# Kernel tuning notes

Measured on AMD Instinct MI355X. Metric: run time of the kernel, lower is better.

Reference implementation:

```python
import jax, jax.numpy as jnp
import numpy as np

NUM_HEADS = 16
HEAD_DIM = 64
NUM_BUCKETS = 32
MAX_DIST = 128
EPS = 1e-5
SCALE = HEAD_DIM ** -0.5


def layer_norm(x, g, b):
    m = jnp.mean(x, axis=-1, keepdims=True)
    v = jnp.mean(jnp.square(x - m), axis=-1, keepdims=True)
    return (x - m) * jax.lax.rsqrt(v + EPS) * g + b


def rel_pos_bias(emb, num_q, num_k):
    # T5-style relative position bucketing (non-causal, bidirectional halves)
    i, j = num_q, num_k
    q_pos = jnp.arange(j - i, j)
    k_pos = jnp.arange(j)
    rel = k_pos[None, :] - q_pos[:, None]  # [i, j]
    nb = NUM_BUCKETS // 2
    ret = (rel >= 0).astype(jnp.int32) * nb
    n = jnp.abs(rel)
    max_exact = nb // 2
    val_large = max_exact + (
        jnp.log(jnp.maximum(n, 1).astype(jnp.float32) / max_exact)
        / np.log(MAX_DIST / max_exact) * (nb - max_exact)
    ).astype(jnp.int32)
    val_large = jnp.minimum(val_large, nb - 1)
    bucket = ret + jnp.where(n < max_exact, n, val_large)
    bias = emb[bucket]                       # [i, j, h]
    return jnp.transpose(bias, (2, 0, 1))[None]  # [1, h, i, j]


def attention(x, ctx, ng, nbv, ncg, ncb, wq, wkv, wo, bo, rel_emb):
    b, n, _ = x.shape
    m = ctx.shape[1]
    xn = layer_norm(x, ng, nbv)
    cn = layer_norm(ctx, ncg, ncb)
    q = xn @ wq                              # [b, n, mid]
    kv = cn @ wkv                            # [b, m, 2*mid]
    k, v = jnp.split(kv, 2, axis=-1)
    def heads(t, L):
        return t.reshape(b, L, NUM_HEADS, HEAD_DIM).transpose(0, 2, 1, 3)
    q, k, v = heads(q, n), heads(k, m), heads(v, m)
    sim = jnp.einsum('bhnd,bhmd->bhnm', q, k)
    sim = (sim + rel_pos_bias(rel_emb, n, m)) * SCALE  # bias added pre-scale (faithful)
    attn = jax.nn.softmax(sim, axis=-1)
    out = jnp.einsum('bhnm,bhmd->bhnd', attn, v)
    out = out.transpose(0, 2, 1, 3).reshape(b, n, NUM_HEADS * HEAD_DIM)
    return out @ wo + bo


def setup_inputs() -> dict:
    key = jax.random.key(0)
    ks = jax.random.split(key, 20)
    F, MID, CF = 1024, NUM_HEADS * HEAD_DIM, 1024
    w = lambda k, shape, s=0.02: jax.random.normal(k, shape, jnp.float32) * s
    inp = {
        'x': jax.random.normal(ks[0], (2, 2048, F), jnp.float32),
        'context': jax.random.normal(ks[1], (2, 512, CF), jnp.float32),
        # self-attention params
        'sa_norm_g': 1.0 + w(ks[2], (F,), 0.1), 'sa_norm_b': w(ks[3], (F,), 0.1),
        'sa_normc_g': 1.0 + w(ks[4], (F,), 0.1), 'sa_normc_b': w(ks[5], (F,), 0.1),
        'sa_wq': w(ks[6], (F, MID)), 'sa_wkv': w(ks[7], (F, 2 * MID)),
        'sa_wo': w(ks[8], (MID, F)), 'sa_bo': w(ks[9], (F,), 0.01),
        'sa_rel': w(ks[10], (NUM_BUCKETS, NUM_HEADS), 0.1),
        # cross-attention params
        'ca_norm_g': 1.0 + w(ks[11], (F,), 0.1), 'ca_norm_b': w(ks[12], (F,), 0.1),
        'ca_normc_g': 1.0 + w(ks[13], (CF,), 0.1), 'ca_normc_b': w(ks[14], (CF,), 0.1),
        'ca_wq': w(ks[15], (F, MID)), 'ca_wkv': w(ks[16], (CF, 2 * MID)),
        'ca_wo': w(ks[17], (MID, F)), 'ca_bo': w(ks[18], (F,), 0.01),
        'ca_rel': w(ks[19], (NUM_BUCKETS, NUM_HEADS), 0.1),
    }
    return inp


def reference(x, context,
              sa_norm_g, sa_norm_b, sa_normc_g, sa_normc_b,
              sa_wq, sa_wkv, sa_wo, sa_bo, sa_rel,
              ca_norm_g, ca_norm_b, ca_normc_g, ca_normc_b,
              ca_wq, ca_wkv, ca_wo, ca_bo, ca_rel):
    # self-attention (context = x, norm_context applied to x)
    x = attention(x, x, sa_norm_g, sa_norm_b, sa_normc_g, sa_normc_b,
                  sa_wq, sa_wkv, sa_wo, sa_bo, sa_rel) + x
    # cross-attention with residual
    x = attention(x, context, ca_norm_g, ca_norm_b, ca_normc_g, ca_normc_b,
                  ca_wq, ca_wkv, ca_wo, ca_bo, ca_rel) + x
    return x
```

## Files before the change

kernel.cpp:

```cpp
#include <hip/hip_runtime.h>
#include <hip/hip_bf16.h>

typedef __hip_bfloat16 bf16;
typedef __attribute__((ext_vector_type(8))) short bf16x8;
typedef __attribute__((ext_vector_type(4))) float f32x4;

__device__ __forceinline__ float b2f(bf16 v) { return __bfloat162float(v); }
__device__ __forceinline__ bf16 f2b(float v) { return __float2bfloat16(v); }

__device__ __forceinline__ float ldx(const void* p, size_t i, bool isb) {
    return isb ? b2f(((const bf16*)p)[i]) : ((const float*)p)[i];
}
__device__ __forceinline__ void stx(void* p, size_t i, bool isb, float v) {
    if (isb) ((bf16*)p)[i] = f2b(v);
    else     ((float*)p)[i] = v;
}
__device__ __forceinline__ void ldx8(const void* p, size_t i, bool isb, float* o) {
    if (isb) {
        const bf16x8 v = *(const bf16x8*)((const bf16*)p + i);
#pragma unroll
        for (int j = 0; j < 8; j++) o[j] = b2f(((const bf16*)&v)[j]);
    } else {
        const float4 v0 = *(const float4*)((const float*)p + i);
        const float4 v1 = *(const float4*)((const float*)p + i + 4);
        o[0]=v0.x; o[1]=v0.y; o[2]=v0.z; o[3]=v0.w;
        o[4]=v1.x; o[5]=v1.y; o[6]=v1.z; o[7]=v1.w;
    }
}

__global__ void sniff_kernel(const void* __restrict__ x, int* __restrict__ flag) {
    const unsigned* w = (const unsigned*)x;
    const int t = threadIdx.x;
    int cnt = 0;
#pragma unroll
    for (int i = 0; i < 4; i++) {
        const unsigned word = w[t * 4 + i];
        const int e = (word >> 23) & 0xFF;
        cnt += (e >= 192) ? 1 : 0;
    }
    __shared__ int red[4];
#pragma unroll
    for (int o = 32; o > 0; o >>= 1) cnt += __shfl_down(cnt, o);
    if ((t & 63) == 0) red[t >> 6] = cnt;
    __syncthreads();
    if (t == 0) flag[0] = ((red[0] + red[1] + red[2] + red[3]) >= 512) ? 1 : 0;
}

__global__ void wconv4_kernel(const void* __restrict__ Wq,
                              const void* __restrict__ Wkv,
                              const void* __restrict__ Wo,
                              bf16* __restrict__ WTq, bf16* __restrict__ WTkv,
                              bf16* __restrict__ WTo,
                              const int* __restrict__ flagp) {
    const bool isb = (*flagp != 0);
    const int z = blockIdx.z;
    const void* W = (z == 0) ? Wq : (z == 3) ? Wo : Wkv;
    bf16* Wt      = (z == 0) ? WTq : (z == 3) ? WTo : WTkv;
    const int N   = (z == 1 || z == 2) ? 2048 : 1024;
    const int K = 1024;
    __shared__ float T[64][65];
    const int n0 = blockIdx.x * 64 + ((z == 2) ? 1024 : 0);
    const int k0 = blockIdx.y * 64;
    const int t = threadIdx.x;
    const int rr = t >> 3, c8 = (t & 7) * 8;
#pragma unroll
    for (int i = 0; i < 2; i++) {
        const int row = rr + i * 32;
        float v[8];
        ldx8(W, (size_t)(k0 + row) * N + n0 + c8, isb, v);
#pragma unroll
        for (int j = 0; j < 8; j++) T[row][c8 + j] = v[j];
    }
    __syncthreads();
#pragma unroll
    for (int i = 0; i < 2; i++) {
        const int row = rr + i * 32;
        bf16x8 ov;
#pragma unroll
        for (int j = 0; j < 8; j++) ((bf16*)&ov)[j] = f2b(T[c8 + j][row]);
        *(bf16x8*)(Wt + (size_t)(n0 + row) * K + k0 + c8) = ov;
    }
}

__global__ void ln_dual_kernel(const void* __restrict__ in, size_t in_off, long in_bs,
                               int in_ext,
                               const void* __restrict__ g1, const void* __restrict__ b1,
                               const void* __restrict__ g2, const void* __restrict__ b2,
                               bf16* __restrict__ out1, bf16* __restrict__ out2,
                               long out_bs, const int* __restrict__ flagp) {
    const int F = 1024;
    const bool isb = (*flagp != 0);
    const bool inb = in_ext ? isb : true;
    const int row = blockIdx.x;
    const int z = blockIdx.z;
    const int t = threadIdx.x;
    const size_t base = in_off + (size_t)z * in_bs + (size_t)row * F;
    const size_t obase = (size_t)z * out_bs + (size_t)row * F;

    float v[4];
    float s = 0.f;
#pragma unroll
    for (int i = 0; i < 4; i++) { v[i] = ldx(in, base + t + 256 * i, inb); s += v[i]; }

    __shared__ float red1[4];
    __shared__ float red2[4];
#pragma unroll
    for (int o = 32; o > 0; o >>= 1) s += __shfl_down(s, o);
    if ((t & 63) == 0) red1[t >> 6] = s;
    __syncthreads();
    const float mean = (red1[0] + red1[1] + red1[2] + red1[3]) * (1.0f / F);

    float ss = 0.f;
#pragma unroll
    for (int i = 0; i < 4; i++) { float d = v[i] - mean; ss += d * d; }
#pragma unroll
    for (int o = 32; o > 0; o >>= 1) ss += __shfl_down(ss, o);
    if ((t & 63) == 0) red2[t >> 6] = ss;
    __syncthreads();
    const float var = (red2[0] + red2[1] + red2[2] + red2[3]) * (1.0f / F);
    const float rn = rsqrtf(var + 1e-5f);

#pragma unroll
    for (int i = 0; i < 4; i++) {
        const int idx = t + 256 * i;
        const float nv = (v[i] - mean) * rn;
        out1[obase + idx] = f2b(nv * ldx(g1, idx, isb) + ldx(b1, idx, isb));
        if (out2) out2[obase + idx] = f2b(nv * ldx(g2, idx, isb) + ldx(b2, idx, isb));
    }
}

__global__ __launch_bounds__(256) void gemm_bt(
    const bf16* __restrict__ A, const bf16* __restrict__ Bt,
    void* __restrict__ C, int c_ext,
    const void* __restrict__ bias,
    const void* __restrict__ res, int res_ext,
    int N, int mode, int zsplit, int zrows,
    bf16* __restrict__ kb0, bf16* __restrict__ kb1,
    const int* __restrict__ flagp) {

    const int K = 1024;
    const bool isb = (*flagp != 0);

    __shared__ bf16 As[128][72];
    __shared__ bf16 Bs[128][72];

    const int t = threadIdx.x;
    const int w = t >> 6, lane = t & 63, li = lane & 15, quad = lane >> 4;
    const int wm = (w & 1) * 64, wn = (w >> 1) * 64;
    const int bm = blockIdx.y * 128, bn = blockIdx.x * 128;

    f32x4 acc[4][4];
#pragma unroll
    for (int mi = 0; mi < 4; mi++)
#pragma unroll
        for (int ni = 0; ni < 4; ni++)
#pragma unroll
            for (int r = 0; r < 4; r++) acc[mi][ni][r] = 0.f;

    for (int k0 = 0; k0 < K; k0 += 64) {
#pragma unroll
        for (int c = 0; c < 4; c++) {
            const int d = c * 256 + t;
            const int row = d >> 3, ch = (d & 7) * 8;
            *(bf16x8*)&As[row][ch] = *(const bf16x8*)(A + (size_t)(bm + row) * K + k0 + ch);
            *(bf16x8*)&Bs[row][ch] = *(const bf16x8*)(Bt + (size_t)(bn + row) * K + k0 + ch);
        }
        __syncthreads();
#pragma unroll
        for (int kc = 0; kc < 2; kc++) {
            bf16x8 af[4], bfr[4];
#pragma unroll
            for (int i = 0; i < 4; i++) {
                af[i]  = *(const bf16x8*)&As[wm + i * 16 + li][kc * 32 + quad * 8];
                bfr[i] = *(const bf16x8*)&Bs[wn + i * 16 + li][kc * 32 + quad * 8];
            }
#pragma unroll
            for (int mi = 0; mi < 4; mi++)
#pragma unroll
                for (int ni = 0; ni < 4; ni++)
                    acc[mi][ni] = __builtin_amdgcn_mfma_f32_16x16x32_bf16(
                        af[mi], bfr[ni], acc[mi][ni], 0, 0, 0);
        }
        __syncthreads();
    }

    if (mode == 1) {
#pragma unroll
        for (int mi = 0; mi < 4; mi++)
#pragma unroll
            for (int r = 0; r < 4; r++) {
                const int row = bm + wm + mi * 16 + quad * 4 + r;
                bf16* kb = (row < zsplit) ? kb0 : kb1;
                const int lrow = (row < zsplit) ? row : row - zsplit;
#pragma unroll
                for (int ni = 0; ni < 4; ni++) {
                    const int col = bn + wn + ni * 16 + li;
                    const float v = acc[mi][ni][r];
                    if (col < 1024)
                        kb[(size_t)lrow * 1024 + col] = f2b(v);
                    else
                        kb[(size_t)1024 * zrows + (size_t)(col - 1024) * zrows + lrow] = f2b(v);
                }
            }
        return;
    }

#pragma unroll
    for (int mi = 0; mi < 4; mi++)
#pragma unroll
        for (int r = 0; r < 4; r++) {
            const int row = bm + wm + mi * 16 + quad * 4 + r;
#pragma unroll
            for (int ni = 0; ni < 4; ni++) {
                const int col = bn + wn + ni * 16 + li;
                float v = acc[mi][ni][r];
                if (bias) v += ldx(bias, col, isb);
                if (res)  v += ldx(res, (size_t)row * N + col, res_ext ? isb : true);
                stx(C, (size_t)row * N + col, c_ext ? isb : true, v);
            }
        }
}

__global__ __launch_bounds__(256) void gemm_mfma(
    const bf16* __restrict__ A, long a_bs, const void* __restrict__ W,
    void* __restrict__ C, size_t c_off, long c_bs, int c_ext,
    const void* __restrict__ bias,
    const void* __restrict__ res, size_t res_off, long res_bs, int res_ext,
    int K, int N, int mode, int R,
    bf16* __restrict__ kb0, bf16* __restrict__ kb1,
    const int* __restrict__ flagp) {

    const bool isb = (*flagp != 0);
    const bool resb = res_ext ? isb : true;
    const bool cb = c_ext ? isb : true;
    const int z = blockIdx.z;

    const bf16* Az = A + (size_t)z * a_bs;
    const size_t coz = c_off + (size_t)z * c_bs;
    const size_t roz = res_off + (size_t)z * res_bs;

    __shared__ bf16 As[64][72];
    __shared__ bf16 Bs[64][72];

    const int t = threadIdx.x;
    const int w = t >> 6, lane = t & 63, li = lane & 15, quad = lane >> 4;
    const int wm = (w & 1) * 32, wn = (w >> 1) * 32;
    const int bm = blockIdx.y * 64, bn = blockIdx.x * 64;

    f32x4 acc[2][2];
#pragma unroll
    for (int mi = 0; mi < 2; mi++)
#pragma unroll
        for (int ni = 0; ni < 2; ni++)
#pragma unroll
            for (int r = 0; r < 4; r++) acc[mi][ni][r] = 0.f;

    for (int k0 = 0; k0 < K; k0 += 64) {
#pragma unroll
        for (int c = 0; c < 2; c++) {
            const int lin = t * 16 + c * 8;
            const int row = lin >> 6, kk = lin & 63;
            *(bf16x8*)&As[row][kk] = *(const bf16x8*)(Az + (size_t)(bm + row) * K + k0 + kk);
        }
#pragma unroll
        for (int c = 0; c < 2; c++) {
            const int lin = t * 16 + c * 8;
            const int kk = lin >> 6, n0 = lin & 63;
            float v[8];
            ldx8(W, (size_t)(k0 + kk) * N + bn + n0, isb, v);
            const int st = t & 7;
#pragma unroll
            for (int i = 0; i < 8; i++) {
                const int ii = (i + st) & 7;
                Bs[n0 + ii][kk] = f2b(v[ii]);
            }
        }
        __syncthreads();
#pragma unroll
        for (int kc = 0; kc < 2; kc++) {
            bf16x8 af[2], bfr[2];
#pragma unroll
            for (int mi = 0; mi < 2; mi++)
                af[mi] = *(const bf16x8*)&As[wm + mi * 16 + li][kc * 32 + quad * 8];
#pragma unroll
            for (int ni = 0; ni < 2; ni++)
                bfr[ni] = *(const bf16x8*)&Bs[wn + ni * 16 + li][kc * 32 + quad * 8];
#pragma unroll
            for (int mi = 0; mi < 2; mi++)
#pragma unroll
                for (int ni = 0; ni < 2; ni++)
                    acc[mi][ni] = __builtin_amdgcn_mfma_f32_16x16x32_bf16(
                        af[mi], bfr[ni], acc[mi][ni], 0, 0, 0);
        }
        __syncthreads();
    }

    if (mode == 1) {
        bf16* kb = z ? kb1 : kb0;
#pragma unroll
        for (int mi = 0; mi < 2; mi++)
#pragma unroll
            for (int r = 0; r < 4; r++) {
                const int row = bm + wm + mi * 16 + quad * 4 + r;
#pragma unroll
                for (int ni = 0; ni < 2; ni++) {
                    const int col = bn + wn + ni * 16 + li;
                    const float v = acc[mi][ni][r];
                    if (col < 1024)
                        kb[(size_t)row * 1024 + col] = f2b(v);
                    else
                        kb[(size_t)1024 * R + (size_t)(col - 1024) * R + row] = f2b(v);
                }
            }
        return;
    }

#pragma unroll
    for (int mi = 0; mi < 2; mi++)
#pragma unroll
        for (int r = 0; r < 4; r++) {
            const int row = bm + wm + mi * 16 + quad * 4 + r;
#pragma unroll
            for (int ni = 0; ni < 2; ni++) {
                const int col = bn + wn + ni * 16 + li;
                float v = acc[mi][ni][r];
                if (bias) v += ldx(bias, col, isb);
                if (res)  v += ldx(res, roz + (size_t)row * N + col, resb);
                stx(C, coz + (size_t)row * N + col, cb, v);
            }
        }
}

__global__ __launch_bounds__(64) void attn_flash(
    const bf16* __restrict__ qb, const bf16* __restrict__ kv0,
    const bf16* __restrict__ kv1,
    const void* __restrict__ rel_emb, bf16* __restrict__ out,
    long qo_bs, long out_bs, int m, int rel_off, const int* __restrict__ flagp) {

    const float SC = 0.125f * 1.44269504f;
    const bool isb = (*flagp != 0);
    const int id = blockIdx.x;
    const int xcd = id & 7;
    const int slot = id >> 3;
    const int c = (slot >> 6) * 8 + xcd;
    const int h = c & 15, z = c >> 4;
    const int q0 = (slot & 63) * 32;
    const int t = threadIdx.x;
    const int li = t & 15, quad = t >> 4;

    const bf16* qz = qb + (size_t)z * qo_bs;
    bf16* oz = out + (size_t)z * out_bs;
    const bf16* kb = z ? kv1 : kv0;
    const bf16* vtb = kb + (size_t)m * 1024;

    __shared__ float bias_s[32];
    __shared__ float tab[2080];
    __shared__ bf16 Ps[16][40];

    if (t < 32) bias_s[t] = ldx(rel_emb, t * 16 + h, isb) * SC - 40.0f;
    __syncthreads();

    const int tsz = m + 31;
    for (int i = t; i < tsz; i += 64) {
        const int rel = i - 31 - q0 + rel_off;
        const int ab = rel < 0 ? -rel : rel;
        int bucket = rel >= 0 ? 16 : 0;
        if (ab < 8) {
            bucket += ab;
        } else {
            const int p = 31 - __clz(ab);
            const int k2 = 2 * p + ((ab * ab >= (1 << (2 * p + 1))) ? 1 : 0);
            const int val = k2 + 2;
            bucket += (val > 15) ? 15 : val;
        }
        tab[i] = bias_s[bucket];
    }
    __syncthreads();

    bf16x8 aq[2][2];
#pragma unroll
    for (int g = 0; g < 2; g++)
#pragma unroll
        for (int kc = 0; kc < 2; kc++)
            aq[g][kc] = *(const bf16x8*)(qz + (size_t)(q0 + g * 16 + li) * 1024
                                         + h * 64 + kc * 32 + quad * 8);

    bf16x8 ones;
#pragma unroll
    for (int j = 0; j < 8; j++) ((short*)&ones)[j] = 0x3F80;

    f32x4 o[2][4], lac[2];
#pragma unroll
    for (int g = 0; g < 2; g++) {
#pragma unroll
        for (int r = 0; r < 4; r++) lac[g][r] = 0.f;
#pragma unroll
        for (int nb = 0; nb < 4; nb++)
#pragma unroll
            for (int r = 0; r < 4; r++) o[g][nb][r] = 0.f;
    }

    for (int j0 = 0; j0 < m; j0 += 32) {
        bf16x8 kf[4], vf[4];
#pragma unroll
        for (int nb = 0; nb < 2; nb++)
#pragma unroll
            for (int kc = 0; kc < 2; kc++)
                kf[nb * 2 + kc] = *(const bf16x8*)(
                    kb + (size_t)(j0 + nb * 16 + li) * 1024 + h * 64 + kc * 32 + quad * 8);
#pragma unroll
        for (int nb = 0; nb < 4; nb++)
            vf[nb] = *(const bf16x8*)(
                vtb + (size_t)(h * 64 + nb * 16 + li) * m + j0 + quad * 8);

#pragma unroll
        for (int g = 0; g < 2; g++) {
            f32x4 s[2];
#pragma unroll
            for (int nb = 0; nb < 2; nb++) {
                f32x4 a;
#pragma unroll
                for (int r = 0; r < 4; r++) a[r] = 0.f;
#pragma unroll
                for (int kc = 0; kc < 2; kc++)
                    a = __builtin_amdgcn_mfma_f32_16x16x32_bf16(aq[g][kc], kf[nb * 2 + kc],
                                                                a, 0, 0, 0);
                s[nb] = a;
            }
#pragma unroll
            for (int nb = 0; nb < 2; nb++)
#pragma unroll
                for (int r = 0; r < 4; r++) {
                    const int ti = j0 + nb * 16 + li + 31 - (g * 16 + quad * 4 + r);
                    s[nb][r] = exp2f(fmaf(s[nb][r], SC, tab[ti]));
                }
#pragma unroll
            for (int nb = 0; nb < 2; nb++)
#pragma unroll
                for (int r = 0; r < 4; r++)
                    Ps[quad * 4 + r][nb * 16 + li] = f2b(s[nb][r]);
            const bf16x8 ap = *(const bf16x8*)&Ps[li][quad * 8];
#pragma unroll
            for (int nb = 0; nb < 4; nb++)
                o[g][nb] = __builtin_amdgcn_mfma_f32_16x16x32_bf16(ap, vf[nb],
                                                                   o[g][nb], 0, 0, 0);
            lac[g] = __builtin_amdgcn_mfma_f32_16x16x32_bf16(ap, ones, lac[g], 0, 0, 0);
        }
    }

#pragma unroll
    for (int g = 0; g < 2; g++)
#pragma unroll
        for (int r = 0; r < 4; r++) {
            const float inv = 1.0f / lac[g][r];
            const int qi = q0 + g * 16 + quad * 4 + r;
#pragma unroll
            for (int nb = 0; nb < 4; nb++)
                oz[(size_t)qi * 1024 + h * 64 + nb * 16 + li] = f2b(o[g][nb][r] * inv);
        }
}

extern "C" void kernel_launch(void* const* d_in, const int* in_sizes, int n_in,
                              void* d_out, int out_size, void* d_ws, size_t ws_size,
                              hipStream_t stream) {
    const long M1 = 1024 * 1024;
    const long M2 = 2 * 1024 * 1024;
    const long M4 = 4 * 1024 * 1024;
    if (ws_size < 24u * 1024 * 1024 + 256) return;

    const void* x      = d_in[0];
    const void* ctx    = d_in[1];
    const void* sa_ng  = d_in[2];
    const void* sa_nb  = d_in[3];
    const void* sa_ncg = d_in[4];
    const void* sa_ncb = d_in[5];
    const void* sa_wq  = d_in[6];
    const void* sa_wkv = d_in[7];
    const void* sa_wo  = d_in[8];
    const void* sa_bo  = d_in[9];
    const void* sa_rel = d_in[10];
    const void* ca_ng  = d_in[11];
    const void* ca_nb  = d_in[12];
    const void* ca_ncg = d_in[13];
    const void* ca_ncb = d_in[14];
    const void* ca_wq  = d_in[15];
    const void* ca_wkv = d_in[16];
    const void* ca_wo  = d_in[17];
    const void* ca_bo  = d_in[18];
    const void* ca_rel = d_in[19];

    int* flag = (int*)d_ws;
    bf16* F_A = (bf16*)((char*)d_ws + 256);
    bf16* F_B = F_A + M4;
    bf16* F_C = F_B + M4;
    bf16* WT  = F_C + M4;
    bf16* qd  = (bf16*)d_out;

    sniff_kernel<<<1, 256, 0, stream>>>(x, flag);

    if (ws_size >= 32u * 1024 * 1024 + 256) {
        bf16* WTq = WT;
        bf16* WTkv = WT + M1;
        bf16* WTo = WT + 3 * M1;

        wconv4_kernel<<<dim3(16, 16, 4), 256, 0, stream>>>(
            sa_wq, sa_wkv, sa_wo, WTq, WTkv, WTo, flag);
        ln_dual_kernel<<<dim3(2048, 1, 2), 256, 0, stream>>>(
            x, 0, M2, 1, sa_ng, sa_nb, sa_ncg, sa_ncb, F_A, F_B, M2, flag);
        gemm_bt<<<dim3(8, 32), 256, 0, stream>>>(
            F_A, WTq, qd, 0, nullptr, nullptr, 0, 1024, 0, 0, 0,
            nullptr, nullptr, flag);
        gemm_bt<<<dim3(16, 32), 256, 0, stream>>>(
            F_B, WTkv, nullptr, 0, nullptr, nullptr, 0, 2048, 1, 2048, 2048,
            F_A, F_C, flag);
        attn_flash<<<dim3(2048), 64, 0, stream>>>(
            qd, F_A, F_C, sa_rel, qd, M2, M2, 2048, 0, flag);
        gemm_bt<<<dim3(8, 32), 256, 0, stream>>>(
            qd, WTo, F_B, 0, sa_bo, x, 1, 1024, 0, 0, 0,
            nullptr, nullptr, flag);

        wconv4_kernel<<<dim3(16, 16, 4), 256, 0, stream>>>(
            ca_wq, ca_wkv, ca_wo, WTq, WTkv, WTo, flag);
        ln_dual_kernel<<<dim3(2048, 1, 2), 256, 0, stream>>>(
            F_B, 0, M2, 0, ca_ng, ca_nb, nullptr, nullptr, F_A, nullptr, M2, flag);
        ln_dual_kernel<<<dim3(512, 1, 2), 256, 0, stream>>>(
            ctx, 0, 512 * 1024, 1, ca_ncg, ca_ncb, nullptr, nullptr,
            F_C, nullptr, 512 * 1024, flag);
        gemm_bt<<<dim3(8, 32), 256, 0, stream>>>(
            F_A, WTq, qd, 0, nullptr, nullptr, 0, 1024, 0, 0, 0,
            nullptr, nullptr, flag);
        gemm_bt<<<dim3(16, 8), 256, 0, stream>>>(
            F_C, WTkv, nullptr, 0, nullptr, nullptr, 0, 2048, 1, 512, 512,
            F_A, F_A + M1, flag);
        attn_flash<<<dim3(2048), 64, 0, stream>>>(
            qd, F_A, F_A + M1, ca_rel, F_C, M2, M2, 512, 1536, flag);
        gemm_bt<<<dim3(8, 32), 256, 0, stream>>>(
            F_C, WTo, d_out, 1, ca_bo, F_B, 0, 1024, 0, 0, 0,
            nullptr, nullptr, flag);
        return;
    }

    ln_dual_kernel<<<dim3(2048, 1, 2), 256, 0, stream>>>(
        x, 0, M2, 1, sa_ng, sa_nb, sa_ncg, sa_ncb, F_A, F_B, M2, flag);
    gemm_mfma<<<dim3(16, 32, 2), 256, 0, stream>>>(
        F_A, M2, sa_wq, qd, 0, M2, 0, nullptr, nullptr, 0, 0, 0,
        1024, 1024, 0, 0, nullptr, nullptr, flag);
    gemm_mfma<<<dim3(32, 32, 2), 256, 0, stream>>>(
        F_B, M2, sa_wkv, nullptr, 0, 0, 0, nullptr, nullptr, 0, 0, 0,
        1024, 2048, 1, 2048, F_A, F_C, flag);
    attn_flash<<<dim3(2048), 64, 0, stream>>>(
        qd, F_A, F_C, sa_rel, qd, M2, M2, 2048, 0, flag);
    gemm_mfma<<<dim3(16, 32, 2), 256, 0, stream>>>(
        qd, M2, sa_wo, F_B, 0, M2, 0, sa_bo, x, 0, M2, 1,
        1024, 1024, 0, 0, nullptr, nullptr, flag);

    ln_dual_kernel<<<dim3(2048, 1, 2), 256, 0, stream>>>(
        F_B, 0, M2, 0, ca_ng, ca_nb, nullptr, nullptr, F_A, nullptr, M2, flag);
    ln_dual_kernel<<<dim3(512, 1, 2), 256, 0, stream>>>(
        ctx, 0, 512 * 1024, 1, ca_ncg, ca_ncb, nullptr, nullptr,
        F_C, nullptr, 512 * 1024, flag);
    gemm_mfma<<<dim3(16, 32, 2), 256, 0, stream>>>(
        F_A, M2, ca_wq, qd, 0, M2, 0, nullptr, nullptr, 0, 0, 0,
        1024, 1024, 0, 0, nullptr, nullptr, flag);
    gemm_mfma<<<dim3(32, 8, 2), 256, 0, stream>>>(
        F_C, 512 * 1024, ca_wkv, nullptr, 0, 0, 0, nullptr, nullptr, 0, 0, 0,
        1024, 2048, 1, 512, F_A, F_A + M1, flag);
    attn_flash<<<dim3(2048), 64, 0, stream>>>(
        qd, F_A, F_A + M1, ca_rel, F_C, M2, M2, 512, 1536, flag);
    gemm_mfma<<<dim3(16, 32, 2), 256, 0, stream>>>(
        F_C, M2, ca_wo, d_out, 0, M2, 1, ca_bo, F_B, 0, M2, 0,
        1024, 1024, 0, 0, nullptr, nullptr, flag);
}
```

Baseline: 510.3 us.

## Split attention key range across two waves per block and combine partial sums

Each attention block now runs two wavefronts, and each wave processes half of the key/value sequence. The unnormalised outputs and row sums are merged through shared memory before wave 0 writes the result. This is safe without a running max because the softmax uses a fixed offset, so partial sums add directly. The aim is more parallelism and latency hiding per query tile at the cost of an extra combine step and more LDS per block. s_setprio hints are also added around the MFMA sections.

```diff
diff --git a/kernel.cpp b/kernel.cpp
--- a/kernel.cpp
+++ b/kernel.cpp
@@ -331,7 +331,7 @@
         }
 }
 
-__global__ __launch_bounds__(64) void attn_flash(
+__global__ __launch_bounds__(128) void attn_flash(
     const bf16* __restrict__ qb, const bf16* __restrict__ kv0,
     const bf16* __restrict__ kv1,
     const void* __restrict__ rel_emb, bf16* __restrict__ out,
@@ -346,22 +346,26 @@
     const int h = c & 15, z = c >> 4;
     const int q0 = (slot & 63) * 32;
     const int t = threadIdx.x;
-    const int li = t & 15, quad = t >> 4;
+    const int w = t >> 6;
+    const int lane = t & 63;
+    const int li = lane & 15, quad = lane >> 4;
 
     const bf16* qz = qb + (size_t)z * qo_bs;
     bf16* oz = out + (size_t)z * out_bs;
     const bf16* kb = z ? kv1 : kv0;
     const bf16* vtb = kb + (size_t)m * 1024;
 
-    __shared__ float bias_s[32];
-    __shared__ float tab[2080];
-    __shared__ bf16 Ps[16][40];
+    __shared__ __align__(16) char smem[11008];
+    float* tab    = (float*)smem;
+    float* bias_s = (float*)(smem + 8320);
+    bf16*  Psw    = (bf16*)(smem + 8448) + w * 640;
+    float* comb   = (float*)smem;
 
     if (t < 32) bias_s[t] = ldx(rel_emb, t * 16 + h, isb) * SC - 40.0f;
     __syncthreads();
 
     const int tsz = m + 31;
-    for (int i = t; i < tsz; i += 64) {
+    for (int i = t; i < tsz; i += 128) {
         const int rel = i - 31 - q0 + rel_off;
         const int ab = rel < 0 ? -rel : rel;
         int bucket = rel >= 0 ? 16 : 0;
@@ -400,7 +404,11 @@
             for (int r = 0; r < 4; r++) o[g][nb][r] = 0.f;
     }
 
-    for (int j0 = 0; j0 < m; j0 += 32) {
+    const int half = m >> 1;
+    const int jbeg = w * half;
+    const int jend = jbeg + half;
+
+    for (int j0 = jbeg; j0 < jend; j0 += 32) {
         bf16x8 kf[4], vf[4];
 #pragma unroll
         for (int nb = 0; nb < 2; nb++)
@@ -416,6 +424,7 @@
 #pragma unroll
         for (int g = 0; g < 2; g++) {
             f32x4 s[2];
+            __builtin_amdgcn_s_setprio(1);
 #pragma unroll
             for (int nb = 0; nb < 2; nb++) {
                 f32x4 a;
@@ -427,6 +436,7 @@
                                                                 a, 0, 0, 0);
                 s[nb] = a;
             }
+            __builtin_amdgcn_s_setprio(0);
 #pragma unroll
             for (int nb = 0; nb < 2; nb++)
 #pragma unroll
@@ -438,26 +448,46 @@
             for (int nb = 0; nb < 2; nb++)
 #pragma unroll
                 for (int r = 0; r < 4; r++)
-                    Ps[quad * 4 + r][nb * 16 + li] = f2b(s[nb][r]);
-            const bf16x8 ap = *(const bf16x8*)&Ps[li][quad * 8];
+                    Psw[(quad * 4 + r) * 40 + nb * 16 + li] = f2b(s[nb][r]);
+            const bf16x8 ap = *(const bf16x8*)&Psw[li * 40 + quad * 8];
+            __builtin_amdgcn_s_setprio(1);
 #pragma unroll
             for (int nb = 0; nb < 4; nb++)
                 o[g][nb] = __builtin_amdgcn_mfma_f32_16x16x32_bf16(ap, vf[nb],
                                                                    o[g][nb], 0, 0, 0);
             lac[g] = __builtin_amdgcn_mfma_f32_16x16x32_bf16(ap, ones, lac[g], 0, 0, 0);
-        }
-    }
-
-#pragma unroll
-    for (int g = 0; g < 2; g++)
-#pragma unroll
-        for (int r = 0; r < 4; r++) {
-            const float inv = 1.0f / lac[g][r];
-            const int qi = q0 + g * 16 + quad * 4 + r;
+            __builtin_amdgcn_s_setprio(0);
+        }
+    }
+
+    __syncthreads();
+    if (w == 1) {
+        float* cl = comb + lane * 41;
+#pragma unroll
+        for (int g = 0; g < 2; g++) {
 #pragma unroll
             for (int nb = 0; nb < 4; nb++)
-                oz[(size_t)qi * 1024 + h * 64 + nb * 16 + li] = f2b(o[g][nb][r] * inv);
-        }
+#pragma unroll
+                for (int r = 0; r < 4; r++) cl[g * 16 + nb * 4 + r] = o[g][nb][r];
+#pragma unroll
+            for (int r = 0; r < 4; r++) cl[32 + g * 4 + r] = lac[g][r];
+        }
+    }
+    __syncthreads();
+    if (w == 0) {
+        const float* cl = comb + lane * 41;
+#pragma unroll
+        for (int g = 0; g < 2; g++)
+#pragma unroll
+            for (int r = 0; r < 4; r++) {
+                const float inv = 1.0f / (lac[g][r] + cl[32 + g * 4 + r]);
+                const int qi = q0 + g * 16 + quad * 4 + r;
+#pragma unroll
+                for (int nb = 0; nb < 4; nb++)
+                    oz[(size_t)qi * 1024 + h * 64 + nb * 16 + li] =
+                        f2b((o[g][nb][r] + cl[g * 16 + nb * 4 + r]) * inv);
+            }
+    }
 }
 
 extern "C" void kernel_launch(void* const* d_in, const int* in_sizes, int n_in,
@@ -513,7 +543,7 @@
         gemm_bt<<<dim3(16, 32), 256, 0, stream>>>(
             F_B, WTkv, nullptr, 0, nullptr, nullptr, 0, 2048, 1, 2048, 2048,
             F_A, F_C, flag);
-        attn_flash<<<dim3(2048), 64, 0, stream>>>(
+        attn_flash<<<dim3(2048), 128, 0, stream>>>(
             qd, F_A, F_C, sa_rel, qd, M2, M2, 2048, 0, flag);
         gemm_bt<<<dim3(8, 32), 256, 0, stream>>>(
             qd, WTo, F_B, 0, sa_bo, x, 1, 1024, 0, 0, 0,
@@ -532,7 +562,7 @@
         gemm_bt<<<dim3(16, 8), 256, 0, stream>>>(
             F_C, WTkv, nullptr, 0, nullptr, nullptr, 0, 2048, 1, 512, 512,
             F_A, F_A + M1, flag);
-        attn_flash<<<dim3(2048), 64, 0, stream>>>(
+        attn_flash<<<dim3(2048), 128, 0, stream>>>(
             qd, F_A, F_A + M1, ca_rel, F_C, M2, M2, 512, 1536, flag);
         gemm_bt<<<dim3(8, 32), 256, 0, stream>>>(
             F_C, WTo, d_out, 1, ca_bo, F_B, 0, 1024, 0, 0, 0,
@@ -548,7 +578,7 @@
     gemm_mfma<<<dim3(32, 32, 2), 256, 0, stream>>>(
         F_B, M2, sa_wkv, nullptr, 0, 0, 0, nullptr, nullptr, 0, 0, 0,
         1024, 2048, 1, 2048, F_A, F_C, flag);
-    attn_flash<<<dim3(2048), 64, 0, stream>>>(
+    attn_flash<<<dim3(2048), 128, 0, stream>>>(
         qd, F_A, F_C, sa_rel, qd, M2, M2, 2048, 0, flag);
     gemm_mfma<<<dim3(16, 32, 2), 256, 0, stream>>>(
         qd, M2, sa_wo, F_B, 0, M2, 0, sa_bo, x, 0, M2, 1,
@@ -565,7 +595,7 @@
     gemm_mfma<<<dim3(32, 8, 2), 256, 0, stream>>>(
         F_C, 512 * 1024, ca_wkv, nullptr, 0, 0, 0, nullptr, nullptr, 0, 0, 0,
         1024, 2048, 1, 512, F_A, F_A + M1, flag);
-    attn_flash<<<dim3(2048), 64, 0, stream>>>(
+    attn_flash<<<dim3(2048), 128, 0, stream>>>(
         qd, F_A, F_A + M1, ca_rel, F_C, M2, M2, 512, 1536, flag);
     gemm_mfma<<<dim3(16, 32, 2), 256, 0, stream>>>(
         F_C, M2, ca_wo, d_out, 0, M2, 1, ca_bo, F_B, 0, M2, 0,
```

Measured after the change: 546.9 us. +7.2%, slower.

## Double-buffer GEMM tiles with direct global-to-LDS async loads

Applied to the files above, without the earlier changes.

The GEMM main loop now stages the next K-tile into a second LDS buffer using global_load_lds (direct global-to-shared DMA) while MFMAs consume the current buffer. This is meant to hide global memory latency and drop the register round-trip of the old load-then-store staging. To suit the DMA layout, the LDS row padding (72) is removed, leaving unpadded 64-wide rows, which can cause bank conflicts on the fragment reads. It also relies on the hardware ordering of the direct loads relative to the single barrier per iteration.

```diff
diff --git a/kernel.cpp b/kernel.cpp
--- a/kernel.cpp
+++ b/kernel.cpp
@@ -26,6 +26,12 @@
         o[0]=v0.x; o[1]=v0.y; o[2]=v0.z; o[3]=v0.w;
         o[4]=v1.x; o[5]=v1.y; o[6]=v1.z; o[7]=v1.w;
     }
+}
+
+__device__ __forceinline__ void glds16(const void* g, void* l) {
+    __builtin_amdgcn_global_load_lds(
+        (const __attribute__((address_space(1))) void*)g,
+        (__attribute__((address_space(3))) void*)l, 16, 0, 0);
 }
 
 __global__ void sniff_kernel(const void* __restrict__ x, int* __restrict__ flag) {
@@ -141,13 +147,15 @@
     const int K = 1024;
     const bool isb = (*flagp != 0);
 
-    __shared__ bf16 As[128][72];
-    __shared__ bf16 Bs[128][72];
+    __shared__ bf16 As[2][128][64];
+    __shared__ bf16 Bs[2][128][64];
 
     const int t = threadIdx.x;
     const int w = t >> 6, lane = t & 63, li = lane & 15, quad = lane >> 4;
     const int wm = (w & 1) * 64, wn = (w >> 1) * 64;
     const int bm = blockIdx.y * 128, bn = blockIdx.x * 128;
+    const int srow = t >> 3;
+    const int sch  = (t & 7) * 8;
 
     f32x4 acc[4][4];
 #pragma unroll
@@ -157,32 +165,50 @@
 #pragma unroll
             for (int r = 0; r < 4; r++) acc[mi][ni][r] = 0.f;
 
-    for (int k0 = 0; k0 < K; k0 += 64) {
-#pragma unroll
-        for (int c = 0; c < 4; c++) {
-            const int d = c * 256 + t;
-            const int row = d >> 3, ch = (d & 7) * 8;
-            *(bf16x8*)&As[row][ch] = *(const bf16x8*)(A + (size_t)(bm + row) * K + k0 + ch);
-            *(bf16x8*)&Bs[row][ch] = *(const bf16x8*)(Bt + (size_t)(bn + row) * K + k0 + ch);
-        }
+#define STAGE(buf, k0)                                                         \
+    {                                                                          \
+        _Pragma("unroll")                                                      \
+        for (int c = 0; c < 4; c++) {                                          \
+            const int row = c * 32 + srow;                                     \
+            glds16(A + (size_t)(bm + row) * K + (k0) + sch,                    \
+                   (char*)&As[buf][0][0] + (size_t)(c * 256 + w * 64) * 16);   \
+            glds16(Bt + (size_t)(bn + row) * K + (k0) + sch,                   \
+                   (char*)&Bs[buf][0][0] + (size_t)(c * 256 + w * 64) * 16);   \
+        }                                                                      \
+    }
+
+#define COMPUTE(buf)                                                           \
+    {                                                                          \
+        _Pragma("unroll")                                                      \
+        for (int kc = 0; kc < 2; kc++) {                                       \
+            bf16x8 af[4], bfr[4];                                              \
+            _Pragma("unroll")                                                  \
+            for (int i = 0; i < 4; i++) {                                      \
+                af[i]  = *(const bf16x8*)&As[buf][wm + i * 16 + li][kc * 32 + quad * 8]; \
+                bfr[i] = *(const bf16x8*)&Bs[buf][wn + i * 16 + li][kc * 32 + quad * 8]; \
+            }                                                                  \
+            _Pragma("unroll")                                                  \
+            for (int mi = 0; mi < 4; mi++)                                     \
+                _Pragma("unroll")                                              \
+                for (int ni = 0; ni < 4; ni++)                                 \
+                    acc[mi][ni] = __builtin_amdgcn_mfma_f32_16x16x32_bf16(     \
+                        af[mi], bfr[ni], acc[mi][ni], 0, 0, 0);                \
+        }                                                                      \
+    }
+
+    STAGE(0, 0);
+    __syncthreads();
+    int cur = 0;
+    for (int k0 = 64; k0 < K; k0 += 64) {
+        STAGE(cur ^ 1, k0);
+        COMPUTE(cur);
         __syncthreads();
-#pragma unroll
-        for (int kc = 0; kc < 2; kc++) {
-            bf16x8 af[4], bfr[4];
-#pragma unroll
-            for (int i = 0; i < 4; i++) {
-                af[i]  = *(const bf16x8*)&As[wm + i * 16 + li][kc * 32 + quad * 8];
-                bfr[i] = *(const bf16x8*)&Bs[wn + i * 16 + li][kc * 32 + quad * 8];
-            }
-#pragma unroll
-            for (int mi = 0; mi < 4; mi++)
-#pragma unroll
-                for (int ni = 0; ni < 4; ni++)
-                    acc[mi][ni] = __builtin_amdgcn_mfma_f32_16x16x32_bf16(
-                        af[mi], bfr[ni], acc[mi][ni], 0, 0, 0);
-        }
-        __syncthreads();
-    }
+        cur ^= 1;
+    }
+    COMPUTE(cur);
+
+#undef STAGE
+#undef COMPUTE
 
     if (mode == 1) {
 #pragma unroll
```

Result: slower. 550.2 us (+7.8%).

## Merge Q and KV projections into one launch; double-buffer K/V loads in attention

Applied to the files above, without the earlier changes.

The Q and KV projection GEMMs now run as a single grouped launch. Each block picks its argument set by blockIdx.x, which fills the GPU better and removes one launch per attention layer. The LN output moves to a new workspace buffer so the KV output no longer aliases it. The flash-attention loop software-pipelines K/V fragment loads across two register sets and raises wave priority around the MFMA sections with s_setprio. The trade-offs are higher register pressure and a larger workspace requirement, so the fast path now needs 40 MB.

```diff
diff --git a/kernel.cpp b/kernel.cpp
--- a/kernel.cpp
+++ b/kernel.cpp
@@ -129,14 +129,20 @@
     }
 }
 
-__global__ __launch_bounds__(256) void gemm_bt(
-    const bf16* __restrict__ A, const bf16* __restrict__ Bt,
-    void* __restrict__ C, int c_ext,
-    const void* __restrict__ bias,
-    const void* __restrict__ res, int res_ext,
-    int N, int mode, int zsplit, int zrows,
-    bf16* __restrict__ kb0, bf16* __restrict__ kb1,
-    const int* __restrict__ flagp) {
+struct GArgs {
+    const bf16* A; const bf16* Bt; void* C;
+    const void* bias; const void* res;
+    bf16* kb0; bf16* kb1;
+    int c_ext, res_ext, N, mode, zsplit, zrows, nbx, nby;
+};
+
+__global__ __launch_bounds__(256) void gemm_fused(GArgs ga, GArgs gb,
+                                                  const int* __restrict__ flagp) {
+    const bool sec = (int)blockIdx.x >= ga.nbx;
+    const GArgs g = sec ? gb : ga;
+    const int bx = (int)blockIdx.x - (sec ? ga.nbx : 0);
+    const int by = (int)blockIdx.y;
+    if (by >= g.nby) return;
 
     const int K = 1024;
     const bool isb = (*flagp != 0);
@@ -147,7 +153,7 @@
     const int t = threadIdx.x;
     const int w = t >> 6, lane = t & 63, li = lane & 15, quad = lane >> 4;
     const int wm = (w & 1) * 64, wn = (w >> 1) * 64;
-    const int bm = blockIdx.y * 128, bn = blockIdx.x * 128;
+    const int bm = by * 128, bn = bx * 128;
 
     f32x4 acc[4][4];
 #pragma unroll
@@ -162,8 +168,8 @@
         for (int c = 0; c < 4; c++) {
             const int d = c * 256 + t;
             const int row = d >> 3, ch = (d & 7) * 8;
-            *(bf16x8*)&As[row][ch] = *(const bf16x8*)(A + (size_t)(bm + row) * K + k0 + ch);
-            *(bf16x8*)&Bs[row][ch] = *(const bf16x8*)(Bt + (size_t)(bn + row) * K + k0 + ch);
+            *(bf16x8*)&As[row][ch] = *(const bf16x8*)(g.A + (size_t)(bm + row) * K + k0 + ch);
+            *(bf16x8*)&Bs[row][ch] = *(const bf16x8*)(g.Bt + (size_t)(bn + row) * K + k0 + ch);
         }
         __syncthreads();
 #pragma unroll
@@ -184,14 +190,14 @@
         __syncthreads();
     }
 
-    if (mode == 1) {
+    if (g.mode == 1) {
 #pragma unroll
         for (int mi = 0; mi < 4; mi++)
 #pragma unroll
             for (int r = 0; r < 4; r++) {
                 const int row = bm + wm + mi * 16 + quad * 4 + r;
-                bf16* kb = (row < zsplit) ? kb0 : kb1;
-                const int lrow = (row < zsplit) ? row : row - zsplit;
+                bf16* kb = (row < g.zsplit) ? g.kb0 : g.kb1;
+                const int lrow = (row < g.zsplit) ? row : row - g.zsplit;
 #pragma unroll
                 for (int ni = 0; ni < 4; ni++) {
                     const int col = bn + wn + ni * 16 + li;
@@ -199,7 +205,7 @@
                     if (col < 1024)
                         kb[(size_t)lrow * 1024 + col] = f2b(v);
                     else
-                        kb[(size_t)1024 * zrows + (size_t)(col - 1024) * zrows + lrow] = f2b(v);
+                        kb[(size_t)1024 * g.zrows + (size_t)(col - 1024) * g.zrows + lrow] = f2b(v);
                 }
             }
         return;
@@ -214,9 +220,9 @@
             for (int ni = 0; ni < 4; ni++) {
                 const int col = bn + wn + ni * 16 + li;
                 float v = acc[mi][ni][r];
-                if (bias) v += ldx(bias, col, isb);
-                if (res)  v += ldx(res, (size_t)row * N + col, res_ext ? isb : true);
-                stx(C, (size_t)row * N + col, c_ext ? isb : true, v);
+                if (g.bias) v += ldx(g.bias, col, isb);
+                if (g.res)  v += ldx(g.res, (size_t)row * g.N + col, g.res_ext ? isb : true);
+                stx(g.C, (size_t)row * g.N + col, g.c_ext ? isb : true, v);
             }
         }
 }
@@ -400,53 +406,76 @@
             for (int r = 0; r < 4; r++) o[g][nb][r] = 0.f;
     }
 
-    for (int j0 = 0; j0 < m; j0 += 32) {
-        bf16x8 kf[4], vf[4];
-#pragma unroll
-        for (int nb = 0; nb < 2; nb++)
-#pragma unroll
-            for (int kc = 0; kc < 2; kc++)
-                kf[nb * 2 + kc] = *(const bf16x8*)(
-                    kb + (size_t)(j0 + nb * 16 + li) * 1024 + h * 64 + kc * 32 + quad * 8);
-#pragma unroll
-        for (int nb = 0; nb < 4; nb++)
-            vf[nb] = *(const bf16x8*)(
-                vtb + (size_t)(h * 64 + nb * 16 + li) * m + j0 + quad * 8);
-
-#pragma unroll
-        for (int g = 0; g < 2; g++) {
-            f32x4 s[2];
-#pragma unroll
-            for (int nb = 0; nb < 2; nb++) {
-                f32x4 a;
-#pragma unroll
-                for (int r = 0; r < 4; r++) a[r] = 0.f;
-#pragma unroll
-                for (int kc = 0; kc < 2; kc++)
-                    a = __builtin_amdgcn_mfma_f32_16x16x32_bf16(aq[g][kc], kf[nb * 2 + kc],
-                                                                a, 0, 0, 0);
-                s[nb] = a;
-            }
-#pragma unroll
-            for (int nb = 0; nb < 2; nb++)
-#pragma unroll
-                for (int r = 0; r < 4; r++) {
-                    const int ti = j0 + nb * 16 + li + 31 - (g * 16 + quad * 4 + r);
-                    s[nb][r] = exp2f(fmaf(s[nb][r], SC, tab[ti]));
-                }
-#pragma unroll
-            for (int nb = 0; nb < 2; nb++)
-#pragma unroll
-                for (int r = 0; r < 4; r++)
-                    Ps[quad * 4 + r][nb * 16 + li] = f2b(s[nb][r]);
-            const bf16x8 ap = *(const bf16x8*)&Ps[li][quad * 8];
-#pragma unroll
-            for (int nb = 0; nb < 4; nb++)
-                o[g][nb] = __builtin_amdgcn_mfma_f32_16x16x32_bf16(ap, vf[nb],
-                                                                   o[g][nb], 0, 0, 0);
-            lac[g] = __builtin_amdgcn_mfma_f32_16x16x32_bf16(ap, ones, lac[g], 0, 0, 0);
-        }
-    }
+#define LOADKV(KF, VF, J)                                                      \
+    {                                                                          \
+        _Pragma("unroll")                                                      \
+        for (int nb = 0; nb < 2; nb++)                                         \
+            _Pragma("unroll")                                                  \
+            for (int kc = 0; kc < 2; kc++)                                     \
+                KF[nb * 2 + kc] = *(const bf16x8*)(                            \
+                    kb + (size_t)((J) + nb * 16 + li) * 1024 + h * 64          \
+                    + kc * 32 + quad * 8);                                     \
+        _Pragma("unroll")                                                      \
+        for (int nb = 0; nb < 4; nb++)                                         \
+            VF[nb] = *(const bf16x8*)(                                         \
+                vtb + (size_t)(h * 64 + nb * 16 + li) * m + (J) + quad * 8);   \
+    }
+
+#define ABODY(KF, VF, J0)                                                      \
+    {                                                                          \
+        _Pragma("unroll")                                                      \
+        for (int g = 0; g < 2; g++) {                                          \
+            f32x4 s[2];                                                        \
+            __builtin_amdgcn_s_setprio(1);                                     \
+            _Pragma("unroll")                                                  \
+            for (int nb = 0; nb < 2; nb++) {                                   \
+                f32x4 a;                                                       \
+                _Pragma("unroll")                                              \
+                for (int r = 0; r < 4; r++) a[r] = 0.f;                        \
+                _Pragma("unroll")                                              \
+                for (int kc = 0; kc < 2; kc++)                                 \
+                    a = __builtin_amdgcn_mfma_f32_16x16x32_bf16(               \
+                        aq[g][kc], KF[nb * 2 + kc], a, 0, 0, 0);               \
+                s[nb] = a;                                                     \
+            }                                                                  \
+            __builtin_amdgcn_s_setprio(0);                                     \
+            _Pragma("unroll")                                                  \
+            for (int nb = 0; nb < 2; nb++)                                     \
+                _Pragma("unroll")                                              \
+                for (int r = 0; r < 4; r++) {                                  \
+                    const int ti = (J0) + nb * 16 + li + 31                    \
+                                   - (g * 16 + quad * 4 + r);                  \
+                    s[nb][r] = exp2f(fmaf(s[nb][r], SC, tab[ti]));             \
+                }                                                              \
+            _Pragma("unroll")                                                  \
+            for (int nb = 0; nb < 2; nb++)                                     \
+                _Pragma("unroll")                                              \
+                for (int r = 0; r < 4; r++)                                    \
+                    Ps[quad * 4 + r][nb * 16 + li] = f2b(s[nb][r]);            \
+            const bf16x8 ap = *(const bf16x8*)&Ps[li][quad * 8];               \
+            __builtin_amdgcn_s_setprio(1);                                     \
+            _Pragma("unroll")                                                  \
+            for (int nb = 0; nb < 4; nb++)                                     \
+                o[g][nb] = __builtin_amdgcn_mfma_f32_16x16x32_bf16(            \
+                    ap, VF[nb], o[g][nb], 0, 0, 0);                            \
+            lac[g] = __builtin_amdgcn_mfma_f32_16x16x32_bf16(                  \
+                ap, ones, lac[g], 0, 0, 0);                                    \
+            __builtin_amdgcn_s_setprio(0);                                     \
+        }                                                                      \
+    }
+
+    bf16x8 kA[4], vA[4], kB[4], vB[4];
+    LOADKV(kA, vA, 0);
+    for (int j0 = 0; j0 < m; j0 += 64) {
+        LOADKV(kB, vB, j0 + 32);
+        ABODY(kA, vA, j0);
+        const int jn = (j0 + 64 < m) ? (j0 + 64) : 0;
+        LOADKV(kA, vA, jn);
+        ABODY(kB, vB, j0 + 32);
+    }
+
+#undef LOADKV
+#undef ABODY
 
 #pragma unroll
     for (int g = 0; g < 2; g++)
@@ -494,49 +523,67 @@
     bf16* F_B = F_A + M4;
     bf16* F_C = F_B + M4;
     bf16* WT  = F_C + M4;
+    bf16* F_X = WT + M4;
     bf16* qd  = (bf16*)d_out;
 
     sniff_kernel<<<1, 256, 0, stream>>>(x, flag);
 
-    if (ws_size >= 32u * 1024 * 1024 + 256) {
+    if (ws_size >= 40u * 1024 * 1024 + 256) {
         bf16* WTq = WT;
         bf16* WTkv = WT + M1;
         bf16* WTo = WT + 3 * M1;
+        GArgs gz = {};
 
         wconv4_kernel<<<dim3(16, 16, 4), 256, 0, stream>>>(
             sa_wq, sa_wkv, sa_wo, WTq, WTkv, WTo, flag);
         ln_dual_kernel<<<dim3(2048, 1, 2), 256, 0, stream>>>(
-            x, 0, M2, 1, sa_ng, sa_nb, sa_ncg, sa_ncb, F_A, F_B, M2, flag);
-        gemm_bt<<<dim3(8, 32), 256, 0, stream>>>(
-            F_A, WTq, qd, 0, nullptr, nullptr, 0, 1024, 0, 0, 0,
-            nullptr, nullptr, flag);
-        gemm_bt<<<dim3(16, 32), 256, 0, stream>>>(
-            F_B, WTkv, nullptr, 0, nullptr, nullptr, 0, 2048, 1, 2048, 2048,
-            F_A, F_C, flag);
+            x, 0, M2, 1, sa_ng, sa_nb, sa_ncg, sa_ncb, F_X, F_B, M2, flag);
+        {
+            GArgs gq = {};
+            gq.A = F_X; gq.Bt = WTq; gq.C = qd;
+            gq.N = 1024; gq.nbx = 8; gq.nby = 32;
+            GArgs gkv = {};
+            gkv.A = F_B; gkv.Bt = WTkv;
+            gkv.N = 2048; gkv.mode = 1; gkv.zsplit = 2048; gkv.zrows = 2048;
+            gkv.kb0 = F_A; gkv.kb1 = F_C; gkv.nbx = 16; gkv.nby = 32;
+            gemm_fused<<<dim3(24, 32), 256, 0, stream>>>(gq, gkv, flag);
+        }
         attn_flash<<<dim3(2048), 64, 0, stream>>>(
             qd, F_A, F_C, sa_rel, qd, M2, M2, 2048, 0, flag);
-        gemm_bt<<<dim3(8, 32), 256, 0, stream>>>(
-            qd, WTo, F_B, 0, sa_bo, x, 1, 1024, 0, 0, 0,
-            nullptr, nullptr, flag);
+        {
+            GArgs go = {};
+            go.A = qd; go.Bt = WTo; go.C = F_B;
+            go.bias = sa_bo; go.res = x; go.res_ext = 1;
+            go.N = 1024; go.nbx = 8; go.nby = 32;
+            gemm_fused<<<dim3(8, 32), 256, 0, stream>>>(go, gz, flag);
+        }
 
         wconv4_kernel<<<dim3(16, 16, 4), 256, 0, stream>>>(
             ca_wq, ca_wkv, ca_wo, WTq, WTkv, WTo, flag);
         ln_dual_kernel<<<dim3(2048, 1, 2), 256, 0, stream>>>(
-            F_B, 0, M2, 0, ca_ng, ca_nb, nullptr, nullptr, F_A, nullptr, M2, flag);
+            F_B, 0, M2, 0, ca_ng, ca_nb, nullptr, nullptr, F_X, nullptr, M2, flag);
         ln_dual_kernel<<<dim3(512, 1, 2), 256, 0, stream>>>(
             ctx, 0, 512 * 1024, 1, ca_ncg, ca_ncb, nullptr, nullptr,
             F_C, nullptr, 512 * 1024, flag);
-        gemm_bt<<<dim3(8, 32), 256, 0, stream>>>(
-            F_A, WTq, qd, 0, nullptr, nullptr, 0, 1024, 0, 0, 0,
-            nullptr, nullptr, flag);
-        gemm_bt<<<dim3(16, 8), 256, 0, stream>>>(
-            F_C, WTkv, nullptr, 0, nullptr, nullptr, 0, 2048, 1, 512, 512,
-            F_A, F_A + M1, flag);
+        {
+            GArgs gq = {};
+            gq.A = F_X; gq.Bt = WTq; gq.C = qd;
+            gq.N = 1024; gq.nbx = 8; gq.nby = 32;
+            GArgs gkv = {};
+            gkv.A = F_C; gkv.Bt = WTkv;
+            gkv.N = 2048; gkv.mode = 1; gkv.zsplit = 512; gkv.zrows = 512;
+            gkv.kb0 = F_A; gkv.kb1 = F_A + M1; gkv.nbx = 16; gkv.nby = 8;
+            gemm_fused<<<dim3(24, 32), 256, 0, stream>>>(gq, gkv, flag);
+        }
         attn_flash<<<dim3(2048), 64, 0, stream>>>(
             qd, F_A, F_A + M1, ca_rel, F_C, M2, M2, 512, 1536, flag);
-        gemm_bt<<<dim3(8, 32), 256, 0, stream>>>(
-            F_C, WTo, d_out, 1, ca_bo, F_B, 0, 1024, 0, 0, 0,
-            nullptr, nullptr, flag);
+        {
+            GArgs go = {};
+            go.A = F_C; go.Bt = WTo; go.C = d_out; go.c_ext = 1;
+            go.bias = ca_bo; go.res = F_B;
+            go.N = 1024; go.nbx = 8; go.nby = 32;
+            gemm_fused<<<dim3(8, 32), 256, 0, stream>>>(go, gz, flag);
+        }
         return;
     }
 
```

New measurement: 503.0 us. No clear change (-1.4%).
